# Performance work log

Measured on AMD Instinct MI355X. Metric: run time of the kernel, lower is better.

## Reference

```python
import jax, jax.numpy as jnp
import numpy as np

S = 14
L_COORD = 5.0
L_NOOBJ = 0.5


def setup_inputs() -> dict:
    key = jax.random.key(0)
    k1, k2, k3 = jax.random.split(key, 3)
    B = 4096
    pred = jax.random.uniform(k1, (B, S, S, 30), dtype=jnp.float32)
    target = jax.random.uniform(k2, (B, S, S, 30), dtype=jnp.float32)
    # matching real YOLO targets where most cells are background.
    gate = jax.random.uniform(k3, (B, S, S))
    conf = jnp.where(gate > 0.85, target[..., 4], 0.0)
    target = target.at[..., 4].set(conf)
    return {"pred_tensor": pred, "target_tensor": target}


def _to_xyxy(b):
    # b: (..., 5) [x, y, w, h, c] -> (..., 4) [x1, y1, x2, y2]
    c = b[..., :2] / 14.0
    half = 0.5 * b[..., 2:4]
    return jnp.concatenate([c - half, c + half], axis=-1)


def _iou_2v1(pbox, tbox):
    # pbox: (B,S,S,2,4) xyxy, tbox: (B,S,S,4) -> iou (B,S,S,2)
    lt = jnp.maximum(pbox[..., :2], tbox[..., None, :2])
    rb = jnp.minimum(pbox[..., 2:], tbox[..., None, 2:])
    wh = jnp.clip(rb - lt, 0.0)
    inter = wh[..., 0] * wh[..., 1]
    a1 = (pbox[..., 2] - pbox[..., 0]) * (pbox[..., 3] - pbox[..., 1])
    a2 = (tbox[..., 2] - tbox[..., 0]) * (tbox[..., 3] - tbox[..., 1])
    return inter / (a1 + a2[..., None] - inter)


def reference(pred_tensor, target_tensor):
    pred, target = pred_tensor, target_tensor
    N = pred.shape[0]
    dt = pred.dtype
    coo = (target[..., 4] > 0).astype(dt)          # (B,S,S) object cells
    noo = 1.0 - coo                                # background cells

    # no-object confidence loss over both conf slots (indices 4 and 9)
    noobj_loss = jnp.sum(noo * ((pred[..., 4] - target[..., 4]) ** 2
                                + (pred[..., 9] - target[..., 9]) ** 2))

    # boxes: (B,S,S,2,5)
    pb = pred[..., :10].reshape(pred.shape[0], S, S, 2, 5)
    tb = target[..., :10].reshape(target.shape[0], S, S, 2, 5)

    # IoU of both predicted boxes vs first target box; detached (torch uses .data)
    iou = jax.lax.stop_gradient(_iou_2v1(_to_xyxy(pb), _to_xyxy(tb[..., 0, :])))
    resp = jax.nn.one_hot(jnp.argmax(iou, axis=-1), 2, dtype=dt)  # (B,S,S,2)
    max_iou = jnp.max(iou, axis=-1)                               # (B,S,S)

    p_resp = jnp.einsum('bijk,bijkc->bijc', resp, pb)  # responsible pred box
    t_resp = jnp.einsum('bijk,bijkc->bijc', resp, tb)  # matching target box
    conf_not_resp = jnp.einsum('bijk,bijk->bij', 1.0 - resp, pb[..., 4])

    contain_loss = jnp.sum(coo * (p_resp[..., 4] - max_iou) ** 2)
    not_contain_loss = jnp.sum(coo * conf_not_resp ** 2)  # target conf forced to 0

    loc_loss = jnp.sum(coo[..., None] * ((p_resp[..., :2] - t_resp[..., :2]) ** 2
               + (jnp.sqrt(p_resp[..., 2:4]) - jnp.sqrt(t_resp[..., 2:4])) ** 2))

    class_loss = jnp.sum(coo[..., None] * (pred[..., 10:] - target[..., 10:]) ** 2)

    total = (L_COORD * loc_loss + contain_loss
             + L_NOOBJ * (noobj_loss + not_contain_loss) + class_loss) / N
    return total
```

## Files before the change

### kernel.cpp

```cpp
#include <hip/hip_runtime.h>


#define CPW 64
#define F4P 480
#define F4C (2 * F4P)
#define LPI 15
#define MAXBLK 1280

__device__ __forceinline__ void gload_lds16(const void* g, void* s) {
    auto g1 = (const __attribute__((address_space(1))) void*)(uintptr_t)g;
    auto s3 = (__attribute__((address_space(3))) void*)(uint32_t)(uintptr_t)s;
    __builtin_amdgcn_global_load_lds(g1, s3, 16, 0, 0);
}

__device__ __forceinline__ float cell_loss(const float* __restrict__ p,
                                           const float* __restrict__ t)
{
    const bool coo = t[4] > 0.0f;
    if (!coo) {
        float d4 = p[4] - t[4];
        float d9 = p[9] - t[9];
        return 0.5f * (d4 * d4 + d9 * d9);
    }
    const float inv14 = 1.0f / 14.0f;
    float p0x1 = p[0]*inv14 - 0.5f*p[2], p0y1 = p[1]*inv14 - 0.5f*p[3];
    float p0x2 = p[0]*inv14 + 0.5f*p[2], p0y2 = p[1]*inv14 + 0.5f*p[3];
    float p1x1 = p[5]*inv14 - 0.5f*p[7], p1y1 = p[6]*inv14 - 0.5f*p[8];
    float p1x2 = p[5]*inv14 + 0.5f*p[7], p1y2 = p[6]*inv14 + 0.5f*p[8];
    float tx1  = t[0]*inv14 - 0.5f*t[2], ty1  = t[1]*inv14 - 0.5f*t[3];
    float tx2  = t[0]*inv14 + 0.5f*t[2], ty2  = t[1]*inv14 + 0.5f*t[3];

    float at = (tx2 - tx1) * (ty2 - ty1);

    float w0 = fmaxf(fminf(p0x2, tx2) - fmaxf(p0x1, tx1), 0.0f);
    float h0 = fmaxf(fminf(p0y2, ty2) - fmaxf(p0y1, ty1), 0.0f);
    float inter0 = w0 * h0;
    float a0 = (p0x2 - p0x1) * (p0y2 - p0y1);
    float iou0 = inter0 / (a0 + at - inter0);

    float w1 = fmaxf(fminf(p1x2, tx2) - fmaxf(p1x1, tx1), 0.0f);
    float h1 = fmaxf(fminf(p1y2, ty2) - fmaxf(p1y1, ty1), 0.0f);
    float inter1 = w1 * h1;
    float a1 = (p1x2 - p1x1) * (p1y2 - p1y1);
    float iou1 = inter1 / (a1 + at - inter1);

    bool  r1      = iou1 > iou0;
    float max_iou = fmaxf(iou0, iou1);

    float prx = r1 ? p[5] : p[0], pry = r1 ? p[6] : p[1];
    float prw = r1 ? p[7] : p[2], prh = r1 ? p[8] : p[3];
    float prc = r1 ? p[9] : p[4];
    float trx = r1 ? t[5] : t[0], try_ = r1 ? t[6] : t[1];
    float trw = r1 ? t[7] : t[2], trh = r1 ? t[8] : t[3];
    float cnr = r1 ? p[4] : p[9];

    float dc = prc - max_iou;
    float contain = dc * dc;
    float not_contain = cnr * cnr;

    float dx = prx - trx, dy = pry - try_;
    float dw = sqrtf(prw) - sqrtf(trw);
    float dh = sqrtf(prh) - sqrtf(trh);
    float loc = dx * dx + dy * dy + dw * dw + dh * dh;

    float cls = 0.0f;
#pragma unroll
    for (int k = 10; k < 30; ++k) {
        float d = p[k] - t[k];
        cls += d * d;
    }
    return 5.0f * loc + contain + 0.5f * not_contain + cls;
}

__global__ __launch_bounds__(64) void yolo_cells(
    const float* __restrict__ pred, const float* __restrict__ targ,
    float* __restrict__ partial, int ncells)
{
    __shared__ float4 smem4[2][F4C];
    const float4* P4 = reinterpret_cast<const float4*>(pred);
    const float4* T4 = reinterpret_cast<const float4*>(targ);

    const int  lane   = threadIdx.x;
    const int  wtiles = (ncells + CPW - 1) / CPW;
    const long maxf4  = (long)ncells * 30 / 4 - 1;

    float acc = 0.0f;
    int tile = blockIdx.x;

    if (tile < wtiles) {
#pragma unroll
        for (int i = 0; i < LPI; ++i) {
            int  j   = i * 64 + lane;
            bool isP = j < F4P;
            long g   = (long)tile * F4P + (isP ? j : j - F4P);
            if (g > maxf4) g = maxf4;
            gload_lds16(isP ? (const void*)(P4 + g) : (const void*)(T4 + g),
                        (void*)&smem4[0][i * 64]);
        }
    }

    int buf = 0;
    for (; tile < wtiles; tile += gridDim.x) {
        int next = tile + gridDim.x;
        if (next < wtiles) {
#pragma unroll
            for (int i = 0; i < LPI; ++i) {
                int  j   = i * 64 + lane;
                bool isP = j < F4P;
                long g   = (long)next * F4P + (isP ? j : j - F4P);
                if (g > maxf4) g = maxf4;
                gload_lds16(isP ? (const void*)(P4 + g) : (const void*)(T4 + g),
                            (void*)&smem4[buf ^ 1][i * 64]);
            }
            asm volatile("s_waitcnt vmcnt(15)" ::: "memory");
        } else {
            asm volatile("s_waitcnt vmcnt(0)" ::: "memory");
        }
        __builtin_amdgcn_sched_barrier(0);

        const float* base = reinterpret_cast<const float*>(&smem4[buf][0]);
        int cell = tile * CPW + lane;
        if (cell < ncells)
            acc += cell_loss(base + lane * 30, base + F4P * 4 + lane * 30);
        buf ^= 1;
    }

#pragma unroll
    for (int off = 32; off > 0; off >>= 1)
        acc += __shfl_down(acc, off, 64);
    if (lane == 0) partial[blockIdx.x] = acc;
}

__global__ __launch_bounds__(256) void yolo_final(
    const float* __restrict__ partial, int n, float* __restrict__ out, float invN)
{
    __shared__ float sm[256];
    float acc = 0.0f;
    for (int i = threadIdx.x; i < n; i += 256) acc += partial[i];
    sm[threadIdx.x] = acc;
    __syncthreads();
#pragma unroll
    for (int s = 128; s > 0; s >>= 1) {
        if (threadIdx.x < s) sm[threadIdx.x] += sm[threadIdx.x + s];
        __syncthreads();
    }
    if (threadIdx.x == 0) out[0] = sm[0] * invN;
}

extern "C" void kernel_launch(void* const* d_in, const int* in_sizes, int n_in,
                              void* d_out, int out_size, void* d_ws, size_t ws_size,
                              hipStream_t stream) {
    const float* pred = (const float*)d_in[0];
    const float* targ = (const float*)d_in[1];
    float* out = (float*)d_out;
    float* partial = (float*)d_ws;

    const int ncells = in_sizes[0] / 30;
    const int B      = ncells / 196;
    const float invN = 1.0f / (float)B;

    const int wtiles  = (ncells + CPW - 1) / CPW;
    const int nblocks = wtiles < MAXBLK ? wtiles : MAXBLK;

    yolo_cells<<<nblocks, 64, 0, stream>>>(pred, targ, partial, ncells);
    yolo_final<<<1, 256, 0, stream>>>(partial, nblocks, out, invN);
}
```

Baseline: 37.13 us.

## Drop LDS double buffering and double the block count for occupancy

Replaces the two-stage LDS prefetch pipeline with a single-buffer load, wait, compute loop. This halves the LDS used per 64-thread block, and the grid cap rises from 1280 to 2560 blocks. The intent is to hide memory latency with more resident waves per CU instead of software prefetching inside each wave. The risk is that each wave now stalls on its own loads, and tail balance across blocks changes.

New measurement: 37.97 us. +2.3%, slower.

```diff
diff --git a/kernel.cpp b/kernel.cpp
--- a/kernel.cpp
+++ b/kernel.cpp
@@ -5,7 +5,7 @@
 #define F4P 480
 #define F4C (2 * F4P)
 #define LPI 15
-#define MAXBLK 1280
+#define NBLOCKS 2560
 
 __device__ __forceinline__ void gload_lds16(const void* g, void* s) {
     auto g1 = (const __attribute__((address_space(1))) void*)(uintptr_t)g;
@@ -76,7 +76,7 @@
     const float* __restrict__ pred, const float* __restrict__ targ,
     float* __restrict__ partial, int ncells)
 {
-    __shared__ float4 smem4[2][F4C];
+    __shared__ float4 smem4[F4C];
     const float4* P4 = reinterpret_cast<const float4*>(pred);
     const float4* T4 = reinterpret_cast<const float4*>(targ);
 
@@ -85,9 +85,8 @@
     const long maxf4  = (long)ncells * 30 / 4 - 1;
 
     float acc = 0.0f;
-    int tile = blockIdx.x;
 
-    if (tile < wtiles) {
+    for (int tile = blockIdx.x; tile < wtiles; tile += gridDim.x) {
 #pragma unroll
         for (int i = 0; i < LPI; ++i) {
             int  j   = i * 64 + lane;
@@ -95,34 +94,15 @@
             long g   = (long)tile * F4P + (isP ? j : j - F4P);
             if (g > maxf4) g = maxf4;
             gload_lds16(isP ? (const void*)(P4 + g) : (const void*)(T4 + g),
-                        (void*)&smem4[0][i * 64]);
+                        (void*)&smem4[i * 64]);
         }
-    }
-
-    int buf = 0;
-    for (; tile < wtiles; tile += gridDim.x) {
-        int next = tile + gridDim.x;
-        if (next < wtiles) {
-#pragma unroll
-            for (int i = 0; i < LPI; ++i) {
-                int  j   = i * 64 + lane;
-                bool isP = j < F4P;
-                long g   = (long)next * F4P + (isP ? j : j - F4P);
-                if (g > maxf4) g = maxf4;
-                gload_lds16(isP ? (const void*)(P4 + g) : (const void*)(T4 + g),
-                            (void*)&smem4[buf ^ 1][i * 64]);
-            }
-            asm volatile("s_waitcnt vmcnt(15)" ::: "memory");
-        } else {
-            asm volatile("s_waitcnt vmcnt(0)" ::: "memory");
-        }
+        asm volatile("s_waitcnt vmcnt(0)" ::: "memory");
         __builtin_amdgcn_sched_barrier(0);
 
-        const float* base = reinterpret_cast<const float*>(&smem4[buf][0]);
+        const float* base = reinterpret_cast<const float*>(&smem4[0]);
         int cell = tile * CPW + lane;
         if (cell < ncells)
             acc += cell_loss(base + lane * 30, base + F4P * 4 + lane * 30);
-        buf ^= 1;
     }
 
 #pragma unroll
@@ -160,7 +140,7 @@
     const float invN = 1.0f / (float)B;
 
     const int wtiles  = (ncells + CPW - 1) / CPW;
-    const int nblocks = wtiles < MAXBLK ? wtiles : MAXBLK;
+    const int nblocks = wtiles < NBLOCKS ? wtiles : NBLOCKS;
 
     yolo_cells<<<nblocks, 64, 0, stream>>>(pred, targ, partial, ncells);
     yolo_final<<<1, 256, 0, stream>>>(partial, nblocks, out, invN);
```
